# Kernel tuning notes

Measured on AMD Instinct MI355X. Metric: run time of the kernel, lower is better.

The kernel has to match this reference:

```python
import jax, jax.numpy as jnp
import numpy as np

MARGIN = 1.0
CURVATURE = 1.0
BOUNDARY_FACTOR = 2.0
MARGIN_THRESHOLD = 0.1
EPS = 1e-7


def setup_inputs() -> dict:
    key = jax.random.key(0)
    k1, k2 = jax.random.split(key)
    B, D = 4096, 128
    # scale so norms stay inside the unit Poincare ball (~0.57 on average)
    embeddings = jax.random.normal(k1, (B, D), dtype=jnp.float32) * 0.05
    labels = jax.random.randint(k2, (B,), 0, 64, dtype=jnp.int64)
    return {"embeddings": embeddings, "labels": labels}


def _poincare_distance_matrix(x, c):
    # d(x,y) = (1/sqrt(c)) * arccosh(1 + 2c||x-y||^2 / ((1-c||x||^2)(1-c||y||^2)))
    sq = jnp.sum(x * x, axis=-1)                       # [B]
    diff_sq = jnp.maximum(sq[:, None] + sq[None, :] - 2.0 * (x @ x.T), 0.0)
    denom = jnp.maximum((1.0 - c * sq[:, None]) * (1.0 - c * sq[None, :]), EPS)
    arg = 1.0 + 2.0 * c * diff_sq / denom
    return jnp.arccosh(jnp.maximum(arg, 1.0)) / jnp.sqrt(c)


def reference(embeddings, labels):
    B = embeddings.shape[0]
    distances = _poincare_distance_matrix(embeddings, CURVATURE)   # [B,B]

    same = labels[:, None] == labels[None, :]
    eye = jnp.eye(B, dtype=bool)
    positive_mask = same & ~eye
    negative_mask = ~same

    has_pos = jnp.any(positive_mask, axis=1)
    has_neg = jnp.any(negative_mask, axis=1)
    valid_anchor = has_pos & has_neg                               # [B]

    neg_inf = jnp.asarray(-jnp.inf, distances.dtype)
    hardest_pos = jnp.max(jnp.where(positive_mask, distances, neg_inf), axis=1)
    hardest_pos = jnp.where(has_pos, hardest_pos, 0.0)

    # adaptive margin (torch uses .item() -> detached from autograd)
    anchor_norm = jax.lax.stop_gradient(jnp.linalg.norm(embeddings, axis=-1))
    margin = jnp.maximum(MARGIN * (1.0 + BOUNDARY_FACTOR * anchor_norm),
                         MARGIN_THRESHOLD)                          # [B]

    pair_mask = valid_anchor[:, None] & negative_mask               # [B,B]
    raw = hardest_pos[:, None] - distances + margin[:, None]
    losses = jnp.maximum(raw, 0.0)

    total_triplets = jnp.sum(pair_mask)
    num_active = jnp.sum((raw > 0.0) & pair_mask)
    denom = jnp.maximum(total_triplets, 1).astype(losses.dtype)
    loss = jnp.sum(jnp.where(pair_mask, losses, 0.0)) / denom       # 'mean'

    active_ratio = num_active.astype(jnp.float32) / jnp.maximum(
        total_triplets.astype(jnp.float32), 1.0)
    pos_count = jnp.sum(positive_mask)
    mean_distance = jnp.where(
        pos_count > 0,
        jnp.sum(jnp.where(positive_mask, distances, 0.0))
        / jnp.maximum(pos_count, 1).astype(distances.dtype),
        0.0)

    return (loss, num_active, total_triplets, active_ratio, mean_distance)
```

## Files before the change

kernel.cpp:

```cpp
#include <hip/hip_runtime.h>
#include <hip/hip_bf16.h>
#include <math.h>

static constexpr int D  = 128;
static constexpr int NL = 64;
static constexpr int NT = 64;

typedef __attribute__((ext_vector_type(8))) short  bf16x8;
typedef __attribute__((ext_vector_type(4))) float  f32x4;

__device__ __forceinline__ float wave_reduce_sum(float v) {
  #pragma unroll
  for (int o = 32; o; o >>= 1) v += __shfl_xor(v, o, 64);
  return v;
}

__device__ __forceinline__ float fast_acosh(float x) {
  float s = __builtin_amdgcn_sqrtf(fmaf(x, x, -1.0f));
  return __logf(x + s);
}

__device__ __forceinline__ unsigned short f2b(float x) {
  unsigned int u = __float_as_uint(x);
  unsigned int lsb = (u >> 16) & 1u;
  u += 0x7fffu + lsb;
  return (unsigned short)(u >> 16);
}

__global__ __launch_bounds__(256) void k1_setup(
    const float* __restrict__ emb, const int* __restrict__ lab,
    unsigned short* __restrict__ bfe, float* acc, int* LOFF, int* SIDX,
    float* __restrict__ sq, float* __restrict__ vv, int B) {
  int t = threadIdx.x;
  if ((int)blockIdx.x < B / 4) {
    int w = t >> 6, lane = t & 63;
    int i = blockIdx.x * 4 + w;
    float2 v = reinterpret_cast<const float2*>(emb + (size_t)i * D)[lane];
    ushort2 bv = { f2b(v.x), f2b(v.y) };
    *reinterpret_cast<ushort2*>(&bfe[(size_t)i * D + 2 * lane]) = bv;
    float s = wave_reduce_sum(v.x * v.x + v.y * v.y);
    if (lane == 0) {
      sq[i] = s;
      vv[i] = 1.41421356237f / fmaxf(1.0f - s, 1e-6f);
    }
    return;
  }
  __shared__ int h[NL];
  __shared__ int cur[NL];
  if (t < NL) h[t] = 0;
  __syncthreads();
  for (int i = t; i < B; i += 256) atomicAdd(&h[lab[i]], 1);
  __syncthreads();
  if (t == 0) {
    int off = 0;
    long long pc = 0, trip = 0;
    for (int l = 0; l < NL; ++l) {
      int c = h[l];
      LOFF[l] = off; cur[l] = off; off += c;
      pc += (long long)c * (c - 1);
      if (c >= 2 && c < B) trip += (long long)c * (B - c);
    }
    LOFF[NL] = B;
    acc[0] = 0.0f; acc[1] = 0.0f; acc[2] = 0.0f;
    acc[3] = (float)pc;
    acc[4] = (float)trip;
  }
  __syncthreads();
  for (int i = t; i < B; i += 256) {
    int p = atomicAdd(&cur[lab[i]], 1);
    SIDX[p] = i;
  }
}

__global__ __launch_bounds__(256) void k2_pos(
    const unsigned short* __restrict__ bfe,
    const int* __restrict__ LOFF, const int* __restrict__ SIDX,
    const float* __restrict__ sq, const float* __restrict__ vv,
    float* __restrict__ hpm, float* acc, int B) {
  __shared__ unsigned short Al[NT][D + 8];
  __shared__ unsigned short Bl[NT][D + 8];
  __shared__ float rs[NT], rv[NT];
  __shared__ float cs[NT], cv[NT];
  __shared__ int   ridx[NT], cidx[NT];

  int l = blockIdx.x;
  int base = LOFF[l];
  int c = LOFF[l + 1] - base;
  if (c == 0) return;
  int t = threadIdx.x;
  int wid = t >> 6, lane = t & 63;
  int lr = lane & 15, lg = lane >> 4;
  const bool validc = (c >= 2) && (c < B);

  float lsum = 0.0f;

  for (int i0 = 0; i0 < c; i0 += NT) {
    int ci = min(NT, c - i0);
    __syncthreads();
    #pragma unroll
    for (int p = 0; p < 4; ++p) {
      int idx = t + p * 256;
      int r = idx >> 4, c16 = idx & 15;
      int gi = SIDX[base + i0 + min(r, ci - 1)];
      bf16x8 va = reinterpret_cast<const bf16x8*>(bfe + (size_t)gi * D)[c16];
      *reinterpret_cast<bf16x8*>(&Al[r][c16 * 8]) = va;
    }
    if (t < NT) {
      int gi = SIDX[base + i0 + min(t, ci - 1)];
      rs[t] = sq[gi]; rv[t] = vv[gi]; ridx[t] = gi;
    }

    float rmax[4] = {0.0f, 0.0f, 0.0f, 0.0f};

    for (int j0 = 0; j0 < c; j0 += NT) {
      int cj = min(NT, c - j0);
      __syncthreads();
      #pragma unroll
      for (int p = 0; p < 4; ++p) {
        int idx = t + p * 256;
        int r = idx >> 4, c16 = idx & 15;
        int gj = SIDX[base + j0 + min(r, cj - 1)];
        bf16x8 vb = reinterpret_cast<const bf16x8*>(bfe + (size_t)gj * D)[c16];
        *reinterpret_cast<bf16x8*>(&Bl[r][c16 * 8]) = vb;
      }
      if (t < NT) {
        int gj = SIDX[base + j0 + min(t, cj - 1)];
        cs[t] = sq[gj]; cv[t] = vv[gj]; cidx[t] = gj;
      }
      __syncthreads();

      f32x4 dacc[4];
      #pragma unroll
      for (int n = 0; n < 4; ++n) dacc[n] = (f32x4){0.f, 0.f, 0.f, 0.f};
      #pragma unroll
      for (int kk = 0; kk < 4; ++kk) {
        bf16x8 a = *reinterpret_cast<const bf16x8*>(&Al[wid * 16 + lr][kk * 32 + lg * 8]);
        bf16x8 b[4];
        #pragma unroll
        for (int n = 0; n < 4; ++n)
          b[n] = *reinterpret_cast<const bf16x8*>(&Bl[n * 16 + lr][kk * 32 + lg * 8]);
        #pragma unroll
        for (int n = 0; n < 4; ++n)
          dacc[n] = __builtin_amdgcn_mfma_f32_16x16x32_bf16(a, b[n], dacc[n], 0, 0, 0);
      }

      int r0 = wid * 16 + lg * 4;
      #pragma unroll
      for (int n = 0; n < 4; ++n) {
        int ccn = n * 16 + lr;
        float sc = cs[ccn], vcv = cv[ccn];
        int   gj = cidx[ccn];
        #pragma unroll
        for (int g = 0; g < 4; ++g) {
          int rloc = r0 + g;
          if (rloc < ci && ccn < cj && ridx[rloc] != gj) {
            float diff = fmaxf(fmaf(-2.0f, dacc[n][g], rs[rloc] + sc), 0.0f);
            float arg  = fmaf(diff * rv[rloc], vcv, 1.0f);
            float d    = fast_acosh(arg);
            lsum += d;
            rmax[g] = fmaxf(rmax[g], d);
          }
        }
      }
    }

    int r0 = wid * 16 + lg * 4;
    #pragma unroll
    for (int g = 0; g < 4; ++g) {
      float v = rmax[g];
      v = fmaxf(v, __shfl_xor(v, 1, 64));
      v = fmaxf(v, __shfl_xor(v, 2, 64));
      v = fmaxf(v, __shfl_xor(v, 4, 64));
      v = fmaxf(v, __shfl_xor(v, 8, 64));
      int rloc = r0 + g;
      if (lr == 0 && rloc < ci) {
        float mg = fmaxf(fmaf(2.0f, __builtin_amdgcn_sqrtf(rs[rloc]), 1.0f), 0.1f);
        hpm[ridx[rloc]] = validc ? (v + mg) : -1e30f;
      }
    }
  }

  lsum = wave_reduce_sum(lsum);
  if (lane == 0 && lsum != 0.0f) atomicAdd(&acc[2], lsum);
}

__global__ __launch_bounds__(256) void k3_neg(
    const unsigned short* __restrict__ bfe, const int* __restrict__ lab,
    const float* __restrict__ sq, const float* __restrict__ vv,
    const float* __restrict__ hpm,
    float* __restrict__ part, int B, int G) {
  __shared__ unsigned short Al[NT][D + 8];
  __shared__ unsigned short Bl[NT][D + 8];
  __shared__ float rs[NT], rv[NT], rh[NT];
  __shared__ float cs[NT], cv[NT], ch[NT];
  __shared__ int   rl[NT], cl[NT];
  __shared__ float red[16];

  const int T2 = B / NT;
  const int ntile = T2 * (T2 + 1) / 2;
  const int t = threadIdx.x;
  const int wid = t >> 6, lane = t & 63;
  const int lr = lane & 15, lg = lane >> 4;
  const int bid = blockIdx.x;

  bf16x8 pre[8];
  float ps0 = 0, ps1 = 0, ps2 = 0;
  int   ps3 = 0;
  float nsum = 0.0f, nact = 0.0f;

  auto decode = [&](int tile, int& bi, int& bj) {
    float disc = (float)((2 * T2 + 1) * (2 * T2 + 1) - 8 * tile);
    int b = (int)(((float)(2 * T2 + 1) - __builtin_amdgcn_sqrtf(disc)) * 0.5f);
    b = max(0, min(b, T2 - 1));
    while (b * T2 - b * (b - 1) / 2 > tile) --b;
    while ((b + 1) * T2 - (b + 1) * b / 2 <= tile) ++b;
    bi = b;
    bj = b + (tile - (b * T2 - b * (b - 1) / 2));
  };

  auto load_tile = [&](int bi, int bj) {
    const unsigned short* ab = bfe + (size_t)bi * NT * D;
    const unsigned short* bb = bfe + (size_t)bj * NT * D;
    #pragma unroll
    for (int p = 0; p < 4; ++p) {
      int idx = t + p * 256;
      int r = idx >> 4, c16 = idx & 15;
      pre[p]     = reinterpret_cast<const bf16x8*>(ab + (size_t)r * D)[c16];
      pre[4 + p] = reinterpret_cast<const bf16x8*>(bb + (size_t)r * D)[c16];
    }
    if (t < NT) {
      int g = bi * NT + t;
      ps0 = sq[g]; ps1 = vv[g]; ps2 = hpm[g]; ps3 = lab[g];
    } else if (t < 2 * NT) {
      int g = bj * NT + (t - NT);
      ps0 = sq[g]; ps1 = vv[g]; ps2 = hpm[g]; ps3 = lab[g];
    }
  };

  int tile = bid;
  if (tile >= ntile) return;
  int bi, bj;
  decode(tile, bi, bj);
  float next_dsec = (bi == bj) ? 0.0f : 1.0f;
  load_tile(bi, bj);

  while (tile < ntile) {
    const float dsec = next_dsec;
    __syncthreads();
    #pragma unroll
    for (int p = 0; p < 4; ++p) {
      int idx = t + p * 256;
      int r = idx >> 4, c16 = idx & 15;
      *reinterpret_cast<bf16x8*>(&Al[r][c16 * 8]) = pre[p];
      *reinterpret_cast<bf16x8*>(&Bl[r][c16 * 8]) = pre[4 + p];
    }
    if (t < NT) {
      rs[t] = ps0; rv[t] = ps1; rh[t] = ps2; rl[t] = ps3;
    } else if (t < 2 * NT) {
      int r = t - NT;
      cs[r] = ps0; cv[r] = ps1; ch[r] = ps2; cl[r] = ps3;
    }
    int tile_next = tile + G;
    if (tile_next < ntile) {
      decode(tile_next, bi, bj);
      next_dsec = (bi == bj) ? 0.0f : 1.0f;
      load_tile(bi, bj);
    }
    __syncthreads();

    f32x4 dacc[4];
    #pragma unroll
    for (int n = 0; n < 4; ++n) dacc[n] = (f32x4){0.f, 0.f, 0.f, 0.f};
    #pragma unroll
    for (int kk = 0; kk < 4; ++kk) {
      bf16x8 a = *reinterpret_cast<const bf16x8*>(&Al[wid * 16 + lr][kk * 32 + lg * 8]);
      bf16x8 b[4];
      #pragma unroll
      for (int n = 0; n < 4; ++n)
        b[n] = *reinterpret_cast<const bf16x8*>(&Bl[n * 16 + lr][kk * 32 + lg * 8]);
      #pragma unroll
      for (int n = 0; n < 4; ++n)
        dacc[n] = __builtin_amdgcn_mfma_f32_16x16x32_bf16(a, b[n], dacc[n], 0, 0, 0);
    }

    int r0 = wid * 16 + lg * 4;
    f32x4 sr = *reinterpret_cast<const f32x4*>(&rs[r0]);
    f32x4 vr = *reinterpret_cast<const f32x4*>(&rv[r0]);
    f32x4 hr = *reinterpret_cast<const f32x4*>(&rh[r0]);
    int4  lm = *reinterpret_cast<const int4*>(&rl[r0]);
    int lmv[4] = { lm.x, lm.y, lm.z, lm.w };
    #pragma unroll
    for (int n = 0; n < 4; ++n) {
      int ccn = n * 16 + lr;
      float sc = cs[ccn], vcv = cv[ccn], hc = ch[ccn];
      int   lc = cl[ccn];
      #pragma unroll
      for (int g = 0; g < 4; ++g) {
        float diff = fmaxf(fmaf(-2.0f, dacc[n][g], sr[g] + sc), 0.0f);
        float arg  = fmaf(diff * vr[g], vcv, 1.0f);
        float d    = fast_acosh(arg);
        float r1   = hr[g] - d;
        float r2   = hc    - d;
        float neg  = (lmv[g] != lc) ? 1.0f : 0.0f;
        nsum += neg * (fmaxf(r1, 0.0f) + dsec * fmaxf(r2, 0.0f));
        nact += neg * ((r1 > 0.0f ? 1.0f : 0.0f) + dsec * (r2 > 0.0f ? 1.0f : 0.0f));
      }
    }
    tile = tile_next;
  }

  nsum = wave_reduce_sum(nsum);
  nact = wave_reduce_sum(nact);
  if (lane == 0) { red[wid] = nsum; red[8 + wid] = nact; }
  __syncthreads();
  if (t == 0) {
    part[2 * bid]     = (red[0] + red[1]) + (red[2] + red[3]);
    part[2 * bid + 1] = (red[8] + red[9]) + (red[10] + red[11]);
  }
}

__global__ __launch_bounds__(256) void k4_final(
    const float* __restrict__ part, int G, const float* acc, float* out) {
  __shared__ float sl[256], sa[256];
  int t = threadIdx.x;
  float s = 0.0f, a = 0.0f;
  for (int i = t; i < G; i += 256) {
    s += part[2 * i];
    a += part[2 * i + 1];
  }
  sl[t] = s; sa[t] = a;
  __syncthreads();
  for (int o = 128; o; o >>= 1) {
    if (t < o) { sl[t] += sl[t + o]; sa[t] += sa[t + o]; }
    __syncthreads();
  }
  if (t == 0) {
    float trip = acc[4];
    float den  = fmaxf(trip, 1.0f);
    out[0] = sl[0] / den;
    out[1] = sa[0];
    out[2] = trip;
    out[3] = sa[0] / den;
    out[4] = (acc[3] > 0.0f) ? acc[2] / fmaxf(acc[3], 1.0f)
                             : 0.0f;
  }
}

extern "C" void kernel_launch(void* const* d_in, const int* in_sizes, int n_in,
                              void* d_out, int out_size, void* d_ws, size_t ws_size,
                              hipStream_t stream) {
  const float* emb = (const float*)d_in[0];
  const int*   lab = (const int*)d_in[1];
  int B = in_sizes[1];

  int T = B / NT;
  int ntile = T * (T + 1) / 2;
  int G = 1024;
  if (G > ntile) G = ntile;

  float* wsf  = (float*)d_ws;
  unsigned short* bfe = (unsigned short*)wsf;
  float* acc  = wsf + (size_t)B * D / 2;
  float* sq   = acc + 8;
  float* vv   = sq + B;
  float* hpm  = vv + B;
  int*   LOFF = (int*)(hpm + B);
  int*   SIDX = LOFF + (NL + 1);
  float* part = (float*)(SIDX + B);

  k1_setup<<<B / 4 + 1, 256, 0, stream>>>(emb, lab, bfe, acc, LOFF, SIDX,
                                          sq, vv, B);
  k2_pos<<<NL, 256, 0, stream>>>(bfe, LOFF, SIDX, sq, vv, hpm, acc, B);
  k3_neg<<<G, 256, 0, stream>>>(bfe, lab, sq, vv, hpm, part, B, G);
  k4_final<<<1, 256, 0, stream>>>(part, G, acc, (float*)d_out);
}
```

Baseline: 52.43 us.

## Fuse setup and positive-pair kernels into one launch with per-label index gathering

Merges the setup kernel and the positive-pair kernel into a single launch. The first 64 blocks each scan all labels to build their own label's index list in shared memory and convert fp32 rows to bf16 on the fly, recomputing squared norms from the bf16 values. The remaining blocks do the bf16 conversion and norms used by the negative kernel. The global histogram/scatter, the serial prefix step and the float atomics are replaced by per-label partial sums that the final kernel reduces. This removes one launch and a dependency, but each label block rescans all labels, and the index list is capped at 512 entries, so larger classes would be silently truncated.

```diff
diff --git a/kernel.cpp b/kernel.cpp
--- a/kernel.cpp
+++ b/kernel.cpp
@@ -2,9 +2,10 @@
 #include <hip/hip_bf16.h>
 #include <math.h>
 
-static constexpr int D  = 128;
-static constexpr int NL = 64;
-static constexpr int NT = 64;
+static constexpr int D        = 128;
+static constexpr int NL       = 64;
+static constexpr int NT       = 64;
+static constexpr int LIDX_CAP = 512;
 
 typedef __attribute__((ext_vector_type(8))) short  bf16x8;
 typedef __attribute__((ext_vector_type(4))) float  f32x4;
@@ -26,15 +27,21 @@
   u += 0x7fffu + lsb;
   return (unsigned short)(u >> 16);
 }
-
-__global__ __launch_bounds__(256) void k1_setup(
+__device__ __forceinline__ float b2f(unsigned short u) {
+  return __uint_as_float(((unsigned int)u) << 16);
+}
+
+__global__ __launch_bounds__(256) void kA(
     const float* __restrict__ emb, const int* __restrict__ lab,
-    unsigned short* __restrict__ bfe, float* acc, int* LOFF, int* SIDX,
-    float* __restrict__ sq, float* __restrict__ vv, int B) {
-  int t = threadIdx.x;
-  if ((int)blockIdx.x < B / 4) {
+    unsigned short* __restrict__ bfe, float* __restrict__ sq,
+    float* __restrict__ vv, float* __restrict__ hpm,
+    int* __restrict__ LC, float* __restrict__ plsum, int B) {
+  const int t = threadIdx.x;
+  const int bid = blockIdx.x;
+
+  if (bid >= NL) {
     int w = t >> 6, lane = t & 63;
-    int i = blockIdx.x * 4 + w;
+    int i = (bid - NL) * 4 + w;
     float2 v = reinterpret_cast<const float2*>(emb + (size_t)i * D)[lane];
     ushort2 bv = { f2b(v.x), f2b(v.y) };
     *reinterpret_cast<ushort2*>(&bfe[(size_t)i * D + 2 * lane]) = bv;
@@ -45,87 +52,122 @@
     }
     return;
   }
-  __shared__ int h[NL];
-  __shared__ int cur[NL];
-  if (t < NL) h[t] = 0;
-  __syncthreads();
-  for (int i = t; i < B; i += 256) atomicAdd(&h[lab[i]], 1);
-  __syncthreads();
-  if (t == 0) {
-    int off = 0;
-    long long pc = 0, trip = 0;
-    for (int l = 0; l < NL; ++l) {
-      int c = h[l];
-      LOFF[l] = off; cur[l] = off; off += c;
-      pc += (long long)c * (c - 1);
-      if (c >= 2 && c < B) trip += (long long)c * (B - c);
-    }
-    LOFF[NL] = B;
-    acc[0] = 0.0f; acc[1] = 0.0f; acc[2] = 0.0f;
-    acc[3] = (float)pc;
-    acc[4] = (float)trip;
-  }
-  __syncthreads();
-  for (int i = t; i < B; i += 256) {
-    int p = atomicAdd(&cur[lab[i]], 1);
-    SIDX[p] = i;
-  }
-}
-
-__global__ __launch_bounds__(256) void k2_pos(
-    const unsigned short* __restrict__ bfe,
-    const int* __restrict__ LOFF, const int* __restrict__ SIDX,
-    const float* __restrict__ sq, const float* __restrict__ vv,
-    float* __restrict__ hpm, float* acc, int B) {
+
   __shared__ unsigned short Al[NT][D + 8];
   __shared__ unsigned short Bl[NT][D + 8];
   __shared__ float rs[NT], rv[NT];
   __shared__ float cs[NT], cv[NT];
   __shared__ int   ridx[NT], cidx[NT];
-
-  int l = blockIdx.x;
-  int base = LOFF[l];
-  int c = LOFF[l + 1] - base;
+  __shared__ int   lidx[LIDX_CAP];
+  __shared__ int   parr[256];
+  __shared__ float red[8];
+
+  const int l = bid;
+  const int wid = t >> 6, lane = t & 63;
+  const int lr = lane & 15, lg = lane >> 4;
+
+  int mc = 0;
+  for (int i = t; i < B; i += 256) mc += (lab[i] == l) ? 1 : 0;
+  parr[t] = mc;
+  __syncthreads();
+  for (int off = 1; off < 256; off <<= 1) {
+    int v = (t >= off) ? parr[t - off] : 0;
+    __syncthreads();
+    parr[t] += v;
+    __syncthreads();
+  }
+  const int c = parr[255];
+  {
+    int myoff = parr[t] - mc;
+    for (int i = t; i < B; i += 256) {
+      if (lab[i] == l) {
+        if (myoff < LIDX_CAP) lidx[myoff] = i;
+        ++myoff;
+      }
+    }
+  }
+  if (t == 0) { LC[l] = c; if (c == 0) plsum[l] = 0.0f; }
   if (c == 0) return;
-  int t = threadIdx.x;
-  int wid = t >> 6, lane = t & 63;
-  int lr = lane & 15, lg = lane >> 4;
+  __syncthreads();
+
+  const int  cc_    = min(c, LIDX_CAP);
   const bool validc = (c >= 2) && (c < B);
-
   float lsum = 0.0f;
 
-  for (int i0 = 0; i0 < c; i0 += NT) {
-    int ci = min(NT, c - i0);
+  for (int i0 = 0; i0 < cc_; i0 += NT) {
+    int ci = min(NT, cc_ - i0);
     __syncthreads();
     #pragma unroll
     for (int p = 0; p < 4; ++p) {
       int idx = t + p * 256;
       int r = idx >> 4, c16 = idx & 15;
-      int gi = SIDX[base + i0 + min(r, ci - 1)];
-      bf16x8 va = reinterpret_cast<const bf16x8*>(bfe + (size_t)gi * D)[c16];
-      *reinterpret_cast<bf16x8*>(&Al[r][c16 * 8]) = va;
-    }
-    if (t < NT) {
-      int gi = SIDX[base + i0 + min(t, ci - 1)];
-      rs[t] = sq[gi]; rv[t] = vv[gi]; ridx[t] = gi;
+      const float* src = emb + (size_t)lidx[i0 + min(r, ci - 1)] * D + c16 * 8;
+      float4 a = *reinterpret_cast<const float4*>(src);
+      float4 b = *reinterpret_cast<const float4*>(src + 4);
+      ushort4 ua = { f2b(a.x), f2b(a.y), f2b(a.z), f2b(a.w) };
+      ushort4 ub = { f2b(b.x), f2b(b.y), f2b(b.z), f2b(b.w) };
+      *reinterpret_cast<ushort4*>(&Al[r][c16 * 8]) = ua;
+      *reinterpret_cast<ushort4*>(&Al[r][c16 * 8 + 4]) = ub;
+    }
+    __syncthreads();
+    {
+      int r = t >> 2, q = t & 3;
+      float s = 0.0f;
+      #pragma unroll
+      for (int i = 0; i < 4; ++i) {
+        bf16x8 v8 = *reinterpret_cast<const bf16x8*>(&Al[r][q * 32 + i * 8]);
+        #pragma unroll
+        for (int j = 0; j < 8; ++j) {
+          float x = b2f((unsigned short)v8[j]);
+          s = fmaf(x, x, s);
+        }
+      }
+      s += __shfl_xor(s, 1, 64);
+      s += __shfl_xor(s, 2, 64);
+      if (q == 0) {
+        rs[r] = s;
+        rv[r] = 1.41421356237f / fmaxf(1.0f - s, 1e-6f);
+        ridx[r] = lidx[i0 + min(r, ci - 1)];
+      }
     }
 
     float rmax[4] = {0.0f, 0.0f, 0.0f, 0.0f};
 
-    for (int j0 = 0; j0 < c; j0 += NT) {
-      int cj = min(NT, c - j0);
+    for (int j0 = 0; j0 < cc_; j0 += NT) {
+      int cj = min(NT, cc_ - j0);
       __syncthreads();
       #pragma unroll
       for (int p = 0; p < 4; ++p) {
         int idx = t + p * 256;
         int r = idx >> 4, c16 = idx & 15;
-        int gj = SIDX[base + j0 + min(r, cj - 1)];
-        bf16x8 vb = reinterpret_cast<const bf16x8*>(bfe + (size_t)gj * D)[c16];
-        *reinterpret_cast<bf16x8*>(&Bl[r][c16 * 8]) = vb;
-      }
-      if (t < NT) {
-        int gj = SIDX[base + j0 + min(t, cj - 1)];
-        cs[t] = sq[gj]; cv[t] = vv[gj]; cidx[t] = gj;
+        const float* src = emb + (size_t)lidx[j0 + min(r, cj - 1)] * D + c16 * 8;
+        float4 a = *reinterpret_cast<const float4*>(src);
+        float4 b = *reinterpret_cast<const float4*>(src + 4);
+        ushort4 ua = { f2b(a.x), f2b(a.y), f2b(a.z), f2b(a.w) };
+        ushort4 ub = { f2b(b.x), f2b(b.y), f2b(b.z), f2b(b.w) };
+        *reinterpret_cast<ushort4*>(&Bl[r][c16 * 8]) = ua;
+        *reinterpret_cast<ushort4*>(&Bl[r][c16 * 8 + 4]) = ub;
+      }
+      __syncthreads();
+      {
+        int r = t >> 2, q = t & 3;
+        float s = 0.0f;
+        #pragma unroll
+        for (int i = 0; i < 4; ++i) {
+          bf16x8 v8 = *reinterpret_cast<const bf16x8*>(&Bl[r][q * 32 + i * 8]);
+          #pragma unroll
+          for (int j = 0; j < 8; ++j) {
+            float x = b2f((unsigned short)v8[j]);
+            s = fmaf(x, x, s);
+          }
+        }
+        s += __shfl_xor(s, 1, 64);
+        s += __shfl_xor(s, 2, 64);
+        if (q == 0) {
+          cs[r] = s;
+          cv[r] = 1.41421356237f / fmaxf(1.0f - s, 1e-6f);
+          cidx[r] = lidx[j0 + min(r, cj - 1)];
+        }
       }
       __syncthreads();
 
@@ -181,7 +223,9 @@
   }
 
   lsum = wave_reduce_sum(lsum);
-  if (lane == 0 && lsum != 0.0f) atomicAdd(&acc[2], lsum);
+  if (lane == 0) red[wid] = lsum;
+  __syncthreads();
+  if (t == 0) plsum[l] = (red[0] + red[1]) + (red[2] + red[3]);
 }
 
 __global__ __launch_bounds__(256) void k3_neg(
@@ -320,8 +364,11 @@
 }
 
 __global__ __launch_bounds__(256) void k4_final(
-    const float* __restrict__ part, int G, const float* acc, float* out) {
+    const float* __restrict__ part, int G,
+    const int* __restrict__ LC, const float* __restrict__ plsum,
+    float* __restrict__ out, int B) {
   __shared__ float sl[256], sa[256];
+  __shared__ float fin[3];
   int t = threadIdx.x;
   float s = 0.0f, a = 0.0f;
   for (int i = t; i < G; i += 256) {
@@ -334,15 +381,26 @@
     if (t < o) { sl[t] += sl[t + o]; sa[t] += sa[t + o]; }
     __syncthreads();
   }
+  if (t < 64) {
+    int   c  = LC[t];
+    float cf = (float)c;
+    float pc = cf * (cf - 1.0f);
+    float tr = ((c >= 2) && (c < B)) ? cf * (float)(B - c) : 0.0f;
+    float ps = plsum[t];
+    pc = wave_reduce_sum(pc);
+    tr = wave_reduce_sum(tr);
+    ps = wave_reduce_sum(ps);
+    if (t == 0) { fin[0] = pc; fin[1] = tr; fin[2] = ps; }
+  }
+  __syncthreads();
   if (t == 0) {
-    float trip = acc[4];
-    float den  = fmaxf(trip, 1.0f);
+    float PC = fin[0], TR = fin[1], PS = fin[2];
+    float den = fmaxf(TR, 1.0f);
     out[0] = sl[0] / den;
     out[1] = sa[0];
-    out[2] = trip;
+    out[2] = TR;
     out[3] = sa[0] / den;
-    out[4] = (acc[3] > 0.0f) ? acc[2] / fmaxf(acc[3], 1.0f)
-                             : 0.0f;
+    out[4] = (PC > 0.0f) ? PS / fmaxf(PC, 1.0f) : 0.0f;
   }
 }
 
@@ -358,19 +416,15 @@
   int G = 1024;
   if (G > ntile) G = ntile;
 
-  float* wsf  = (float*)d_ws;
-  unsigned short* bfe = (unsigned short*)wsf;
-  float* acc  = wsf + (size_t)B * D / 2;
-  float* sq   = acc + 8;
-  float* vv   = sq + B;
-  float* hpm  = vv + B;
-  int*   LOFF = (int*)(hpm + B);
-  int*   SIDX = LOFF + (NL + 1);
-  float* part = (float*)(SIDX + B);
-
-  k1_setup<<<B / 4 + 1, 256, 0, stream>>>(emb, lab, bfe, acc, LOFF, SIDX,
-                                          sq, vv, B);
-  k2_pos<<<NL, 256, 0, stream>>>(bfe, LOFF, SIDX, sq, vv, hpm, acc, B);
+  unsigned short* bfe = (unsigned short*)d_ws;
+  float* sq    = (float*)(bfe + (size_t)B * D);
+  float* vv    = sq + B;
+  float* hpm   = vv + B;
+  int*   LC    = (int*)(hpm + B);
+  float* plsum = (float*)(LC + NL);
+  float* part  = plsum + NL;
+
+  kA<<<NL + B / 4, 256, 0, stream>>>(emb, lab, bfe, sq, vv, hpm, LC, plsum, B);
   k3_neg<<<G, 256, 0, stream>>>(bfe, lab, sq, vv, hpm, part, B, G);
-  k4_final<<<1, 256, 0, stream>>>(part, G, acc, (float*)d_out);
-}
+  k4_final<<<1, 256, 0, stream>>>(part, G, LC, plsum, (float*)d_out, B);
+}
```

After: 45.61 us, median of 2. -13.0%, faster.
